# Optimization experiments

Hardware: AMD Instinct MI355X
Metric: run time of the kernel (lower is better)

## Reference

```python
import jax, jax.numpy as jnp
import numpy as np

B, T, C = 4, 2048, 1024
H = 16
D = C // H  # head_dim = 64


def setup_inputs() -> dict:
    key = jax.random.key(0)
    ks = jax.random.split(key, 9)
    s = 1.0 / np.sqrt(C)
    return {
        "x": jax.random.normal(ks[0], (B, T, C), dtype=jnp.float32),
        "Wk": jax.random.uniform(ks[1], (C, C), jnp.float32, -s, s),
        "bk": jax.random.uniform(ks[2], (C,), jnp.float32, -s, s),
        "Wq": jax.random.uniform(ks[3], (C, C), jnp.float32, -s, s),
        "bq": jax.random.uniform(ks[4], (C,), jnp.float32, -s, s),
        "Wv": jax.random.uniform(ks[5], (C, C), jnp.float32, -s, s),
        "bv": jax.random.uniform(ks[6], (C,), jnp.float32, -s, s),
        "Wp": jax.random.uniform(ks[7], (C, C), jnp.float32, -s, s),
        "bp": jax.random.uniform(ks[8], (C,), jnp.float32, -s, s),
    }


def reference(x, Wk, bk, Wq, bq, Wv, bv, Wp, bp):
    # projections -> (B, H, T, D)
    def split_heads(y):
        return y.reshape(B, T, H, D).transpose(0, 2, 1, 3)

    k = split_heads(x @ Wk.T + bk)
    q = split_heads(x @ Wq.T + bq)
    v = split_heads(x @ Wv.T + bv)

    att = jnp.einsum("bhtd,bhsd->bhts", q, k) / np.sqrt(D).astype(np.float32)
    causal = jnp.tril(jnp.ones((T, T), dtype=bool))
    att = jnp.where(causal, att, -jnp.inf)
    att = jax.nn.softmax(att, axis=-1)

    y = jnp.einsum("bhts,bhsd->bhtd", att, v)  # (B,H,T,D)
    y = y.transpose(0, 2, 1, 3).reshape(B, T, C)
    return y @ Wp.T + bp
```

## Files before the change

kernel.cpp:

```cpp
#include <hip/hip_runtime.h>
#include <hip/hip_bf16.h>

typedef unsigned short u16;
typedef unsigned int u32;
typedef short short8 __attribute__((ext_vector_type(8)));
typedef short short4v __attribute__((ext_vector_type(4)));
typedef float f32x4 __attribute__((ext_vector_type(4)));

#define MFMA16(a, b, c) __builtin_amdgcn_mfma_f32_16x16x32_bf16((a), (b), (c), 0, 0, 0)

constexpr int kB = 4, kT = 2048, kC = 1024, kH = 16, kD = 64;
constexpr int kBT = kB * kT;
constexpr long kQKV = (long)kB * kH * kT * kD;
constexpr float kSC = 0.125f * 1.4426950408889634f;

__device__ inline u16 f2bf(float f) {
    __hip_bfloat16 h = __float2bfloat16(f);
    return *reinterpret_cast<u16*>(&h);
}
__device__ inline u32 pkbf_trunc(float lo, float hi) {
    return __builtin_amdgcn_perm(__builtin_bit_cast(u32, hi),
                                 __builtin_bit_cast(u32, lo), 0x07060302u);
}
__device__ inline u32 pkbf_rne(float lo, float hi) {
    return ((u32)f2bf(hi) << 16) | (u32)f2bf(lo);
}

__device__ inline void cp16(const u16* g, u16* l) {
    __builtin_amdgcn_global_load_lds(
        (const __attribute__((address_space(1))) unsigned int*)g,
        (__attribute__((address_space(3))) unsigned int*)l, 16, 0, 0);
}

__global__ __launch_bounds__(256) void cast_kernel(
    const float* __restrict__ x,  const float* __restrict__ Wk,
    const float* __restrict__ Wq, const float* __restrict__ Wv,
    const float* __restrict__ Wp,
    u16* __restrict__ xb, u16* __restrict__ wkb, u16* __restrict__ wqb,
    u16* __restrict__ wvb, u16* __restrict__ wpb)
{
    const long id = (long)blockIdx.x * 256 + threadIdx.x;
    const float* src;
    u16* dst;
    long off;
    if (id < 2097152) {
        src = x; dst = xb; off = id;
    } else {
        const long w = (id - 2097152) >> 18;
        off = (id - 2097152) & 262143;
        src = (w == 0) ? Wk : (w == 1) ? Wq : (w == 2) ? Wv : Wp;
        dst = (w == 0) ? wkb : (w == 1) ? wqb : (w == 2) ? wvb : wpb;
    }
    f32x4 v = *(const f32x4*)&src[off * 4];
    short4v s = {(short)f2bf(v[0]), (short)f2bf(v[1]),
                 (short)f2bf(v[2]), (short)f2bf(v[3])};
    *(short4v*)&dst[off * 4] = s;
}

__global__ __launch_bounds__(256) void qkv_gemm_bf16(
    const u16* __restrict__ xb,
    const u16* __restrict__ wkb, const u16* __restrict__ wqb,
    const u16* __restrict__ wvb,
    const float* __restrict__ bk, const float* __restrict__ bq,
    const float* __restrict__ bv,
    u16* __restrict__ kw, u16* __restrict__ qw, u16* __restrict__ vw)
{
    __shared__ u16 As[128 * 32];
    __shared__ u16 Bs[128 * 32];
    const int tid = threadIdx.x;
    const int lane = tid & 63;
    const int wid = tid >> 6;
    const int l15 = lane & 15;
    const int quad = lane >> 4;
    const int m0 = blockIdx.x * 128;
    const int n0 = blockIdx.y * 128;
    const int z = blockIdx.z;

    const u16* W = (z == 0) ? wkb : (z == 1) ? wqb : wvb;
    const float* bias = (z == 0) ? bk : (z == 1) ? bq : bv;

    f32x4 zero = {0.f, 0.f, 0.f, 0.f};
    f32x4 acc[4][4];
#pragma unroll
    for (int i = 0; i < 4; ++i)
#pragma unroll
        for (int j = 0; j < 4; ++j) acc[i][j] = zero;

    const int wm = (wid & 1) * 64;
    const int wn = (wid >> 1) * 64;

    const int sRow = tid >> 2;
    const int sCol = (tid & 3) * 8;
    const int ldsOff = sRow * 32 + sCol;

    for (int k0 = 0; k0 < kC; k0 += 32) {
        cp16(&xb[(long)(m0 + sRow) * kC + k0 + sCol],      &As[ldsOff]);
        cp16(&xb[(long)(m0 + 64 + sRow) * kC + k0 + sCol], &As[64 * 32 + ldsOff]);
        cp16(&W[(long)(n0 + sRow) * kC + k0 + sCol],       &Bs[ldsOff]);
        cp16(&W[(long)(n0 + 64 + sRow) * kC + k0 + sCol],  &Bs[64 * 32 + ldsOff]);
        __syncthreads();
        short8 af[4], bfr[4];
#pragma unroll
        for (int mt = 0; mt < 4; ++mt)
            af[mt] = *(const short8*)&As[(wm + mt * 16 + l15) * 32 + quad * 8];
#pragma unroll
        for (int nt = 0; nt < 4; ++nt)
            bfr[nt] = *(const short8*)&Bs[(wn + nt * 16 + l15) * 32 + quad * 8];
#pragma unroll
        for (int mt = 0; mt < 4; ++mt)
#pragma unroll
            for (int nt = 0; nt < 4; ++nt)
                acc[mt][nt] = MFMA16(af[mt], bfr[nt], acc[mt][nt]);
        __syncthreads();
    }

    const float scale = (z == 1) ? kSC : 1.0f;
#pragma unroll
    for (int nt = 0; nt < 4; ++nt) {
        const int n = n0 + wn + nt * 16 + l15;
        const float bias_f = bias[n];
        const int h = n >> 6, d = n & 63;
#pragma unroll
        for (int mt = 0; mt < 4; ++mt) {
#pragma unroll
            for (int r = 0; r < 4; ++r) {
                const int m = m0 + wm + mt * 16 + quad * 4 + r;
                const int b = m >> 11, t = m & 2047;
                const float v = (acc[mt][nt][r] + bias_f) * scale;
                const int bh = b * kH + h;
                if (z == 2) {
                    vw[((long)bh * kD + d) * kT + t] = f2bf(v);
                } else {
                    u16* dst = (z == 0) ? kw : qw;
                    dst[((long)bh * kT + t) * kD + d] = f2bf(v);
                }
            }
        }
    }
}

__global__ __launch_bounds__(256) void qkv_gemm_kernel(
    const float* __restrict__ x,
    const float* __restrict__ Wk, const float* __restrict__ bk,
    const float* __restrict__ Wq, const float* __restrict__ bq,
    const float* __restrict__ Wv, const float* __restrict__ bv,
    u16* __restrict__ kw, u16* __restrict__ qw, u16* __restrict__ vw)
{
    __shared__ u16 As[128 * 32];
    __shared__ u16 Bs[128 * 32];
    const int tid = threadIdx.x;
    const int lane = tid & 63;
    const int wid = tid >> 6;
    const int l15 = lane & 15;
    const int quad = lane >> 4;
    const int m0 = blockIdx.x * 128;
    const int n0 = blockIdx.y * 128;
    const int z = blockIdx.z;

    const float* W = (z == 0) ? Wk : (z == 1) ? Wq : Wv;
    const float* bias = (z == 0) ? bk : (z == 1) ? bq : bv;

    f32x4 zero = {0.f, 0.f, 0.f, 0.f};
    f32x4 acc[4][4];
#pragma unroll
    for (int i = 0; i < 4; ++i)
#pragma unroll
        for (int j = 0; j < 4; ++j) acc[i][j] = zero;

    const int wm = (wid & 1) * 64;
    const int wn = (wid >> 1) * 64;
    const int row4 = tid >> 3;
    const int col4 = (tid & 7) * 4;

    for (int k0 = 0; k0 < kC; k0 += 32) {
#pragma unroll
        for (int p = 0; p < 4; ++p) {
            const int r = p * 32 + row4;
            f32x4 xa = *(const f32x4*)&x[(long)(m0 + r) * kC + k0 + col4];
            f32x4 wa = *(const f32x4*)&W[(long)(n0 + r) * kC + k0 + col4];
            short4v xs = {(short)f2bf(xa[0]), (short)f2bf(xa[1]),
                          (short)f2bf(xa[2]), (short)f2bf(xa[3])};
            short4v wsv = {(short)f2bf(wa[0]), (short)f2bf(wa[1]),
                           (short)f2bf(wa[2]), (short)f2bf(wa[3])};
            *(short4v*)&As[r * 32 + col4] = xs;
            *(short4v*)&Bs[r * 32 + col4] = wsv;
        }
        __syncthreads();
        short8 af[4], bfr[4];
#pragma unroll
        for (int mt = 0; mt < 4; ++mt)
            af[mt] = *(const short8*)&As[(wm + mt * 16 + l15) * 32 + quad * 8];
#pragma unroll
        for (int nt = 0; nt < 4; ++nt)
            bfr[nt] = *(const short8*)&Bs[(wn + nt * 16 + l15) * 32 + quad * 8];
#pragma unroll
        for (int mt = 0; mt < 4; ++mt)
#pragma unroll
            for (int nt = 0; nt < 4; ++nt)
                acc[mt][nt] = MFMA16(af[mt], bfr[nt], acc[mt][nt]);
        __syncthreads();
    }

    const float scale = (z == 1) ? kSC : 1.0f;
#pragma unroll
    for (int nt = 0; nt < 4; ++nt) {
        const int n = n0 + wn + nt * 16 + l15;
        const float bias_f = bias[n];
        const int h = n >> 6, d = n & 63;
#pragma unroll
        for (int mt = 0; mt < 4; ++mt) {
#pragma unroll
            for (int r = 0; r < 4; ++r) {
                const int m = m0 + wm + mt * 16 + quad * 4 + r;
                const int b = m >> 11, t = m & 2047;
                const float v = (acc[mt][nt][r] + bias_f) * scale;
                const int bh = b * kH + h;
                if (z == 2) {
                    vw[((long)bh * kD + d) * kT + t] = f2bf(v);
                } else {
                    u16* dst = (z == 0) ? kw : qw;
                    dst[((long)bh * kT + t) * kD + d] = f2bf(v);
                }
            }
        }
    }
}

__global__ __launch_bounds__(256) void attn_kernel(
    const u16* qw, const u16* kw, const u16* vw, u16* ow)
{
    __shared__ u16 Ks[2][64 * 64];
    __shared__ u16 VT[2][64 * 64];
    __shared__ u16 Pb[64 * 64];

    const int tid = threadIdx.x;
    const int lane = tid & 63;
    const int wid = tid >> 6;
    const int l15 = lane & 15;
    const int quad = lane >> 4;
    const int id = blockIdx.x;
    const int bh = id & 63;
    const int pr = id >> 6;

    const float NEG = -1.0e30f;
    f32x4 zero = {0.f, 0.f, 0.f, 0.f};
    const short8 onesf = {(short)0x3F80, (short)0x3F80, (short)0x3F80, (short)0x3F80,
                          (short)0x3F80, (short)0x3F80, (short)0x3F80, (short)0x3F80};

    const int r0 = tid >> 3;
    const int cc = tid & 7;
    const int r1 = r0 + 32;
    const int sw0 = r0 * 64 + ((cc ^ (r0 & 7)) * 8);
    const int sw1 = r1 * 64 + ((cc ^ (r1 & 7)) * 8);
    const int c0e = cc * 8;

    const int rl7 = l15 & 7;

    const u16* kbase = kw + (long)bh * kT * kD;
    const u16* vbase = vw + (long)bh * kD * kT;

#pragma unroll
    for (int ph = 0; ph < 2; ++ph) {
        const int qt64 = ph ? (31 - pr) : pr;
        const int tw = qt64 * 64 + wid * 16;

        short8 qf0, qf1;
        {
            const u16* qp = qw + ((long)bh * kT + tw + l15) * kD;
            qf0 = *(const short8*)&qp[quad * 8];
            qf1 = *(const short8*)&qp[32 + quad * 8];
        }

        f32x4 oacc[4];
#pragma unroll
        for (int mo = 0; mo < 4; ++mo) oacc[mo] = zero;
        f32x4 lsum = zero;

        const int n_st = qt64 + 1;

        const u16* kp0 = kbase + (long)r0 * kD + c0e;
        const u16* kp1 = kbase + (long)r1 * kD + c0e;
        const u16* vp0 = vbase + (long)r0 * kT + c0e;
        const u16* vp1 = vbase + (long)r1 * kT + c0e;
        short8 ka = *(const short8*)kp0;
        short8 kb = *(const short8*)kp1;
        short8 va = *(const short8*)vp0;
        short8 vb = *(const short8*)vp1;
        kp0 += 64 * kD; kp1 += 64 * kD;
        vp0 += 64;      vp1 += 64;
        __syncthreads();
        *(short8*)&Ks[0][sw0] = ka;
        *(short8*)&Ks[0][sw1] = kb;
        *(short8*)&VT[0][sw0] = va;
        *(short8*)&VT[0][sw1] = vb;
        if (n_st > 1) {
            ka = *(const short8*)kp0;
            kb = *(const short8*)kp1;
            va = *(const short8*)vp0;
            vb = *(const short8*)vp1;
            kp0 += 64 * kD; kp1 += 64 * kD;
            vp0 += 64;      vp1 += 64;
        }

        for (int st = 0; st < n_st; ++st) {
            __syncthreads();
            const int cur = st & 1;
            if (st + 1 < n_st) {
                const int nxt = cur ^ 1;
                *(short8*)&Ks[nxt][sw0] = ka;
                *(short8*)&Ks[nxt][sw1] = kb;
                *(short8*)&VT[nxt][sw0] = va;
                *(short8*)&VT[nxt][sw1] = vb;
            }
            if (st + 2 < n_st) {
                ka = *(const short8*)kp0;
                kb = *(const short8*)kp1;
                va = *(const short8*)vp0;
                vb = *(const short8*)vp1;
                kp0 += 64 * kD; kp1 += 64 * kD;
                vp0 += 64;      vp1 += 64;
            }

            short8 kf[4][2];
#pragma unroll
            for (int ms = 0; ms < 4; ++ms) {
                const int row = ms * 16 + l15;
#pragma unroll
                for (int k2 = 0; k2 < 2; ++k2)
                    kf[ms][k2] = *(const short8*)
                        &Ks[cur][row * 64 + (((k2 * 4 + quad) ^ rl7) * 8)];
            }
            f32x4 sacc[4];
#pragma unroll
            for (int ms = 0; ms < 4; ++ms) {
                sacc[ms] = MFMA16(kf[ms][0], qf0, zero);
                sacc[ms] = MFMA16(kf[ms][1], qf1, sacc[ms]);
            }

            if (st == n_st - 1) {
                const int tl = wid * 16 + l15;
#pragma unroll
                for (int ms = 0; ms < 4; ++ms)
#pragma unroll
                    for (int r = 0; r < 4; ++r)
                        if (ms * 16 + quad * 4 + r > tl) sacc[ms][r] = NEG;
            }

            const int prow = wid * 16 + l15;
#pragma unroll
            for (int ms = 0; ms < 4; ++ms) {
                const float p0 = exp2f(sacc[ms][0]);
                const float p1 = exp2f(sacc[ms][1]);
                const float p2 = exp2f(sacc[ms][2]);
                const float p3 = exp2f(sacc[ms][3]);
                uint2 pk;
                pk.x = pkbf_trunc(p0, p1);
                pk.y = pkbf_trunc(p2, p3);
                const int chunk = (ms * 2 + (quad >> 1)) ^ rl7;
                *(uint2*)&Pb[prow * 64 + chunk * 8 + (quad & 1) * 4] = pk;
            }

            short8 pf0 = *(const short8*)&Pb[prow * 64 + ((quad ^ rl7) * 8)];
            short8 pf1 = *(const short8*)&Pb[prow * 64 + (((4 + quad) ^ rl7) * 8)];
            lsum = MFMA16(onesf, pf0, lsum);
            lsum = MFMA16(onesf, pf1, lsum);
#pragma unroll
            for (int mo = 0; mo < 4; ++mo) {
                const int row = mo * 16 + l15;
                short8 vf0 = *(const short8*)
                    &VT[cur][row * 64 + ((quad ^ rl7) * 8)];
                short8 vf1 = *(const short8*)
                    &VT[cur][row * 64 + (((4 + quad) ^ rl7) * 8)];
                oacc[mo] = MFMA16(vf0, pf0, oacc[mo]);
                oacc[mo] = MFMA16(vf1, pf1, oacc[mo]);
            }
        }

        const float inv = 1.0f / lsum[0];
        const int t = tw + l15;
        u16* op = ow + ((long)bh * kT + t) * kD;
#pragma unroll
        for (int mo = 0; mo < 4; ++mo) {
            uint2 ov;
            ov.x = pkbf_rne(oacc[mo][0] * inv, oacc[mo][1] * inv);
            ov.y = pkbf_rne(oacc[mo][2] * inv, oacc[mo][3] * inv);
            *(uint2*)&op[mo * 16 + quad * 4] = ov;
        }
    }
}

__global__ __launch_bounds__(256) void out_gemm_bf16(
    const u16* __restrict__ ob, const u16* __restrict__ wpb,
    const float* __restrict__ bp, float* __restrict__ out)
{
    __shared__ u16 As[128 * 32];
    __shared__ u16 Bs[128 * 32];
    const int tid = threadIdx.x;
    const int lane = tid & 63;
    const int wid = tid >> 6;
    const int l15 = lane & 15;
    const int quad = lane >> 4;
    const int m0 = blockIdx.x * 128;
    const int n0 = blockIdx.y * 128;

    f32x4 zero = {0.f, 0.f, 0.f, 0.f};
    f32x4 acc[4][4];
#pragma unroll
    for (int i = 0; i < 4; ++i)
#pragma unroll
        for (int j = 0; j < 4; ++j) acc[i][j] = zero;

    const int wm = (wid & 1) * 64;
    const int wn = (wid >> 1) * 64;

    const int sRow = tid >> 2;
    const int sCol = (tid & 3) * 8;
    const int ldsOff = sRow * 32 + sCol;

    for (int k0 = 0; k0 < kC; k0 += 32) {
        const int h = k0 >> 6;
        const int d = (k0 & 63) + sCol;
        {
            const int m = m0 + sRow, b = m >> 11, t = m & 2047;
            cp16(&ob[(((long)b * kH + h) * kT + t) * kD + d], &As[ldsOff]);
        }
        {
            const int m = m0 + 64 + sRow, b = m >> 11, t = m & 2047;
            cp16(&ob[(((long)b * kH + h) * kT + t) * kD + d], &As[64 * 32 + ldsOff]);
        }
        cp16(&wpb[(long)(n0 + sRow) * kC + k0 + sCol],      &Bs[ldsOff]);
        cp16(&wpb[(long)(n0 + 64 + sRow) * kC + k0 + sCol], &Bs[64 * 32 + ldsOff]);
        __syncthreads();
        short8 af[4], bfr[4];
#pragma unroll
        for (int mt = 0; mt < 4; ++mt)
            af[mt] = *(const short8*)&As[(wm + mt * 16 + l15) * 32 + quad * 8];
#pragma unroll
        for (int nt = 0; nt < 4; ++nt)
            bfr[nt] = *(const short8*)&Bs[(wn + nt * 16 + l15) * 32 + quad * 8];
#pragma unroll
        for (int mt = 0; mt < 4; ++mt)
#pragma unroll
            for (int nt = 0; nt < 4; ++nt)
                acc[mt][nt] = MFMA16(af[mt], bfr[nt], acc[mt][nt]);
        __syncthreads();
    }

#pragma unroll
    for (int nt = 0; nt < 4; ++nt) {
        const int n = n0 + wn + nt * 16 + l15;
        const float bias_f = bp[n];
#pragma unroll
        for (int mt = 0; mt < 4; ++mt) {
#pragma unroll
            for (int r = 0; r < 4; ++r) {
                const int m = m0 + wm + mt * 16 + quad * 4 + r;
                out[(long)m * kC + n] = acc[mt][nt][r] + bias_f;
            }
        }
    }
}

__global__ __launch_bounds__(256) void out_gemm_kernel(
    const u16* __restrict__ ow, const float* __restrict__ Wp,
    const float* __restrict__ bp, float* __restrict__ out)
{
    __shared__ u16 As[128 * 32];
    __shared__ u16 Bs[128 * 32];
    const int tid = threadIdx.x;
    const int lane = tid & 63;
    const int wid = tid >> 6;
    const int l15 = lane & 15;
    const int quad = lane >> 4;
    const int m0 = blockIdx.x * 128;
    const int n0 = blockIdx.y * 128;

    f32x4 zero = {0.f, 0.f, 0.f, 0.f};
    f32x4 acc[4][4];
#pragma unroll
    for (int i = 0; i < 4; ++i)
#pragma unroll
        for (int j = 0; j < 4; ++j) acc[i][j] = zero;

    const int wm = (wid & 1) * 64;
    const int wn = (wid >> 1) * 64;

    const int r0 = tid >> 2;
    const int kkA = (tid & 3) * 8;
    const int r1 = r0 + 64;
    const int row4 = tid >> 3;
    const int col4 = (tid & 7) * 4;

    for (int k0 = 0; k0 < kC; k0 += 32) {
        {
            const int m = m0 + r0, b = m >> 11, t = m & 2047;
            const int kk = k0 + kkA, h = kk >> 6, d = kk & 63;
            *(short8*)&As[r0 * 32 + kkA] =
                *(const short8*)&ow[(((long)b * kH + h) * kT + t) * kD + d];
        }
        {
            const int m = m0 + r1, b = m >> 11, t = m & 2047;
            const int kk = k0 + kkA, h = kk >> 6, d = kk & 63;
            *(short8*)&As[r1 * 32 + kkA] =
                *(const short8*)&ow[(((long)b * kH + h) * kT + t) * kD + d];
        }
#pragma unroll
        for (int p = 0; p < 4; ++p) {
            const int r = p * 32 + row4;
            f32x4 wa = *(const f32x4*)&Wp[(long)(n0 + r) * kC + k0 + col4];
            short4v wsv = {(short)f2bf(wa[0]), (short)f2bf(wa[1]),
                           (short)f2bf(wa[2]), (short)f2bf(wa[3])};
            *(short4v*)&Bs[r * 32 + col4] = wsv;
        }
        __syncthreads();
        short8 af[4], bfr[4];
#pragma unroll
        for (int mt = 0; mt < 4; ++mt)
            af[mt] = *(const short8*)&As[(wm + mt * 16 + l15) * 32 + quad * 8];
#pragma unroll
        for (int nt = 0; nt < 4; ++nt)
            bfr[nt] = *(const short8*)&Bs[(wn + nt * 16 + l15) * 32 + quad * 8];
#pragma unroll
        for (int mt = 0; mt < 4; ++mt)
#pragma unroll
            for (int nt = 0; nt < 4; ++nt)
                acc[mt][nt] = MFMA16(af[mt], bfr[nt], acc[mt][nt]);
        __syncthreads();
    }

#pragma unroll
    for (int nt = 0; nt < 4; ++nt) {
        const int n = n0 + wn + nt * 16 + l15;
        const float bias_f = bp[n];
#pragma unroll
        for (int mt = 0; mt < 4; ++mt) {
#pragma unroll
            for (int r = 0; r < 4; ++r) {
                const int m = m0 + wm + mt * 16 + quad * 4 + r;
                out[(long)m * kC + n] = acc[mt][nt][r] + bias_f;
            }
        }
    }
}

extern "C" void kernel_launch(void* const* d_in, const int* in_sizes, int n_in,
                              void* d_out, int out_size, void* d_ws, size_t ws_size,
                              hipStream_t stream) {
    const float* x  = (const float*)d_in[0];
    const float* Wk = (const float*)d_in[1];
    const float* bk = (const float*)d_in[2];
    const float* Wq = (const float*)d_in[3];
    const float* bq = (const float*)d_in[4];
    const float* Wv = (const float*)d_in[5];
    const float* bv = (const float*)d_in[6];
    const float* Wp = (const float*)d_in[7];
    const float* bp = (const float*)d_in[8];
    float* out = (float*)d_out;

    u16* ws = (u16*)d_ws;
    const size_t kNeed = 72ull * 1024 * 1024;

    if (ws_size >= kNeed) {
        u16* k_ws = ws;
        u16* q_ws = ws + kQKV;
        u16* v_ws = ws + 2 * kQKV;
        u16* xb   = ws + 3 * kQKV;
        u16* o_ws = xb;
        u16* wkb  = ws + 4 * kQKV;
        u16* wqb  = wkb + (long)kC * kC;
        u16* wvb  = wqb + (long)kC * kC;
        u16* wpb  = wvb + (long)kC * kC;

        cast_kernel<<<12288, 256, 0, stream>>>(x, Wk, Wq, Wv, Wp,
                                               xb, wkb, wqb, wvb, wpb);
        qkv_gemm_bf16<<<dim3(kBT / 128, kC / 128, 3), 256, 0, stream>>>(
            xb, wkb, wqb, wvb, bk, bq, bv, k_ws, q_ws, v_ws);
        attn_kernel<<<1024, 256, 0, stream>>>(q_ws, k_ws, v_ws, o_ws);
        out_gemm_bf16<<<dim3(kBT / 128, kC / 128), 256, 0, stream>>>(
            o_ws, wpb, bp, out);
    } else {
        u16* k_ws = ws;
        u16* q_ws = ws + kQKV;
        u16* v_ws = ws + 2 * kQKV;
        u16* o_ws = q_ws;

        qkv_gemm_kernel<<<dim3(kBT / 128, kC / 128, 3), 256, 0, stream>>>(
            x, Wk, bk, Wq, bq, Wv, bv, k_ws, q_ws, v_ws);
        attn_kernel<<<1024, 256, 0, stream>>>(q_ws, k_ws, v_ws, o_ws);
        out_gemm_kernel<<<dim3(kBT / 128, kC / 128), 256, 0, stream>>>(
            o_ws, Wp, bp, out);
    }
}
```

Baseline: 280.6 us.

## Load K and V MFMA fragments directly from global memory, dropping LDS staging

Removes the double-buffered LDS staging of K and V tiles in the attention kernel, along with the per-tile block barriers. Each wave now reads its K and V MFMA fragments straight from global memory, relying on L1/L2 caching because all four waves read the same tiles. This cuts LDS traffic and synchronization but quadruples global and cache load requests and loses the explicit prefetch overlap, so load latency may be exposed.

```diff
diff --git a/kernel.cpp b/kernel.cpp
--- a/kernel.cpp
+++ b/kernel.cpp
@@ -229,8 +229,6 @@
 __global__ __launch_bounds__(256) void attn_kernel(
     const u16* qw, const u16* kw, const u16* vw, u16* ow)
 {
-    __shared__ u16 Ks[2][64 * 64];
-    __shared__ u16 VT[2][64 * 64];
     __shared__ u16 Pb[64 * 64];
 
     const int tid = threadIdx.x;
@@ -247,17 +245,13 @@
     const short8 onesf = {(short)0x3F80, (short)0x3F80, (short)0x3F80, (short)0x3F80,
                           (short)0x3F80, (short)0x3F80, (short)0x3F80, (short)0x3F80};
 
-    const int r0 = tid >> 3;
-    const int cc = tid & 7;
-    const int r1 = r0 + 32;
-    const int sw0 = r0 * 64 + ((cc ^ (r0 & 7)) * 8);
-    const int sw1 = r1 * 64 + ((cc ^ (r1 & 7)) * 8);
-    const int c0e = cc * 8;
-
     const int rl7 = l15 & 7;
 
     const u16* kbase = kw + (long)bh * kT * kD;
     const u16* vbase = vw + (long)bh * kD * kT;
+
+    const u16* kfp = kbase + (long)l15 * kD + quad * 8;
+    const u16* vfp = vbase + (long)l15 * kT + quad * 8;
 
 #pragma unroll
     for (int ph = 0; ph < 2; ++ph) {
@@ -277,64 +271,29 @@
         f32x4 lsum = zero;
 
         const int n_st = qt64 + 1;
-
-        const u16* kp0 = kbase + (long)r0 * kD + c0e;
-        const u16* kp1 = kbase + (long)r1 * kD + c0e;
-        const u16* vp0 = vbase + (long)r0 * kT + c0e;
-        const u16* vp1 = vbase + (long)r1 * kT + c0e;
-        short8 ka = *(const short8*)kp0;
-        short8 kb = *(const short8*)kp1;
-        short8 va = *(const short8*)vp0;
-        short8 vb = *(const short8*)vp1;
-        kp0 += 64 * kD; kp1 += 64 * kD;
-        vp0 += 64;      vp1 += 64;
-        __syncthreads();
-        *(short8*)&Ks[0][sw0] = ka;
-        *(short8*)&Ks[0][sw1] = kb;
-        *(short8*)&VT[0][sw0] = va;
-        *(short8*)&VT[0][sw1] = vb;
-        if (n_st > 1) {
-            ka = *(const short8*)kp0;
-            kb = *(const short8*)kp1;
-            va = *(const short8*)vp0;
-            vb = *(const short8*)vp1;
-            kp0 += 64 * kD; kp1 += 64 * kD;
-            vp0 += 64;      vp1 += 64;
-        }
-
         for (int st = 0; st < n_st; ++st) {
-            __syncthreads();
-            const int cur = st & 1;
-            if (st + 1 < n_st) {
-                const int nxt = cur ^ 1;
-                *(short8*)&Ks[nxt][sw0] = ka;
-                *(short8*)&Ks[nxt][sw1] = kb;
-                *(short8*)&VT[nxt][sw0] = va;
-                *(short8*)&VT[nxt][sw1] = vb;
-            }
-            if (st + 2 < n_st) {
-                ka = *(const short8*)kp0;
-                kb = *(const short8*)kp1;
-                va = *(const short8*)vp0;
-                vb = *(const short8*)vp1;
-                kp0 += 64 * kD; kp1 += 64 * kD;
-                vp0 += 64;      vp1 += 64;
-            }
+            const int s0 = st * 64;
 
             short8 kf[4][2];
 #pragma unroll
             for (int ms = 0; ms < 4; ++ms) {
-                const int row = ms * 16 + l15;
-#pragma unroll
-                for (int k2 = 0; k2 < 2; ++k2)
-                    kf[ms][k2] = *(const short8*)
-                        &Ks[cur][row * 64 + (((k2 * 4 + quad) ^ rl7) * 8)];
+                const u16* kr = kfp + (long)(s0 + ms * 16) * kD;
+                kf[ms][0] = *(const short8*)kr;
+                kf[ms][1] = *(const short8*)(kr + 32);
             }
             f32x4 sacc[4];
 #pragma unroll
             for (int ms = 0; ms < 4; ++ms) {
                 sacc[ms] = MFMA16(kf[ms][0], qf0, zero);
                 sacc[ms] = MFMA16(kf[ms][1], qf1, sacc[ms]);
+            }
+
+            short8 vf[4][2];
+#pragma unroll
+            for (int mo = 0; mo < 4; ++mo) {
+                const u16* vr = vfp + (long)(mo * 16) * kT + s0;
+                vf[mo][0] = *(const short8*)vr;
+                vf[mo][1] = *(const short8*)(vr + 32);
             }
 
             if (st == n_st - 1) {
@@ -366,13 +325,8 @@
             lsum = MFMA16(onesf, pf1, lsum);
 #pragma unroll
             for (int mo = 0; mo < 4; ++mo) {
-                const int row = mo * 16 + l15;
-                short8 vf0 = *(const short8*)
-                    &VT[cur][row * 64 + ((quad ^ rl7) * 8)];
-                short8 vf1 = *(const short8*)
-                    &VT[cur][row * 64 + (((4 + quad) ^ rl7) * 8)];
-                oacc[mo] = MFMA16(vf0, pf0, oacc[mo]);
-                oacc[mo] = MFMA16(vf1, pf1, oacc[mo]);
+                oacc[mo] = MFMA16(vf[mo][0], pf0, oacc[mo]);
+                oacc[mo] = MFMA16(vf[mo][1], pf1, oacc[mo]);
             }
         }
 
```

Measured after the change: 437.8 us. 1.56x slower.
